# Kernel tuning notes

Hardware: AMD Instinct MI355X
Metric: run time of the kernel (lower is better)

The kernel has to match this reference:

```python
import jax, jax.numpy as jnp
import numpy as np

N = 16384        # num_nodes (64 graphs x 256 nodes, consecutive blocks)
G = 64           # num_graphs = len(nodes_per_graph)
GENES = 12132    # num_genes (hardcoded in source)
E = 262144       # edges, avg degree 16
PER = 256        # nodes per graph


def setup_inputs() -> dict:
    key = jax.random.key(0)
    ks = jax.random.split(key, 12)
    x = jax.random.normal(ks[0], (N, GENES), dtype=jnp.float32)
    edge_index = jax.random.randint(ks[1], (2, E), 0, N, dtype=jnp.int32)
    # node i belongs to graph i // PER  (consecutive-block partition as in the source loop)
    graph_ids = jnp.repeat(jnp.arange(G, dtype=jnp.int32), PER)
    node_scales = jax.random.uniform(ks[2], (GENES,), dtype=jnp.float32, minval=0.5, maxval=1.5)
    gcn_weight = jax.random.normal(ks[3], (GENES, G), dtype=jnp.float32) / np.float32(np.sqrt(GENES))
    gcn_bias = jax.random.normal(ks[4], (G,), dtype=jnp.float32) * 0.01
    w1 = jax.random.normal(ks[5], (G, N), dtype=jnp.float32) / np.float32(np.sqrt(N))   # to_graph_layer [out,in]
    b1 = jax.random.normal(ks[6], (G,), dtype=jnp.float32) * 0.01
    final_means = jax.random.normal(ks[7], (G,), dtype=jnp.float32)
    final_scales = jax.random.uniform(ks[8], (G,), dtype=jnp.float32, minval=0.5, maxval=1.5)
    w2 = jax.random.normal(ks[9], (1, G), dtype=jnp.float32) / np.float32(np.sqrt(G))   # to_final_layer
    b2 = jax.random.normal(ks[10], (1,), dtype=jnp.float32) * 0.01
    return {
        "x": x, "edge_index": edge_index, "graph_ids": graph_ids,
        "node_scales": node_scales, "gcn_weight": gcn_weight, "gcn_bias": gcn_bias,
        "w1": w1, "b1": b1, "final_means": final_means, "final_scales": final_scales,
        "w2": w2, "b2": b2,
    }


def reference(x, edge_index, graph_ids, node_scales, gcn_weight, gcn_bias,
              w1, b1, final_means, final_scales, w2, b2):
    n = x.shape[0]
    x = x / node_scales                              # [N, GENES]
    xw = x @ gcn_weight                              # [N, G]  GCNConv linear (normalize=False)
    src, dst = edge_index[0], edge_index[1]
    # message passing: sum x_j over in-edges; '+ xw' realizes the explicitly-added self loops
    agg = jax.ops.segment_sum(xw[src], dst, num_segments=n) + xw + gcn_bias  # [N, G]
    # per-graph gather: node i takes column graph_ids[i] (vectorized form of the source loop)
    selected = jnp.take_along_axis(agg, graph_ids[:, None], axis=1)[:, 0]    # [N]
    # NOTE: the (selected - graph_means)/graph_scales in the source is dead code
    # (immediately overwritten by `x = selected_outputs`), so it is omitted.
    h = w1 @ selected + b1                           # [G]
    h = (h - final_means) / final_scales
    out = w2 @ h + b2                                # [1]
    return jax.nn.sigmoid(out)
```

## Files before the change

kernel.cpp:

```cpp
#include <hip/hip_runtime.h>
#include <hip/hip_bf16.h>

typedef unsigned short u16;
typedef unsigned int   u32;
typedef __attribute__((ext_vector_type(8))) short bf16x8;
typedef __attribute__((ext_vector_type(4))) float f32x4;
typedef __attribute__((ext_vector_type(4))) u32   u32x4;

#define GENES  12132
#define KPAD   12160
#define NROW   16384
#define GCOL   64
#define KTAIL  12096
#define KSPLIT 10
#define CPW    38

__device__ __forceinline__ u32 pack_hi(float x, float y) {
  return __builtin_amdgcn_perm(__float_as_uint(y), __float_as_uint(x), 0x07060302u);
}
__device__ __forceinline__ u32 pack_lo(float x, float y) {
  float lx = x - __uint_as_float(__float_as_uint(x) & 0xFFFF0000u);
  float ly = y - __uint_as_float(__float_as_uint(y) & 0xFFFF0000u);
  return pack_hi(lx, ly);
}
__device__ __forceinline__ void cvt8v(f32x4 a, f32x4 b, bf16x8& h8, bf16x8& l8) {
  u32x4 hv = { pack_hi(a[0], a[1]), pack_hi(a[2], a[3]),
               pack_hi(b[0], b[1]), pack_hi(b[2], b[3]) };
  u32x4 lv = { pack_lo(a[0], a[1]), pack_lo(a[2], a[3]),
               pack_lo(b[0], b[1]), pack_lo(b[2], b[3]) };
  h8 = __builtin_bit_cast(bf16x8, hv);
  l8 = __builtin_bit_cast(bf16x8, lv);
}

__global__ __launch_bounds__(256) void prep_all(
    const float* __restrict__ gw, const float* __restrict__ ns,
    const float* __restrict__ x,
    u16* __restrict__ B2, float* __restrict__ xpad, float* __restrict__ hbuf) {
  const int bid = blockIdx.x;
  const int t   = threadIdx.x;
  if (bid < KPAD / 64) {
    __shared__ u16 th[64 * 72];
    __shared__ u16 tl[64 * 72];
    const int k0 = bid * 64;
#pragma unroll
    for (int i = 0; i < 16; ++i) {
      int idx = i * 256 + t;
      int k = idx >> 6, c = idx & 63;
      int gk = k0 + k;
      float wv = 0.f;
      if (gk < GENES) wv = gw[(size_t)gk * GCOL + c] / ns[gk];
      u32 u = __float_as_uint(wv);
      float lf = wv - __uint_as_float(u & 0xFFFF0000u);
      th[c * 72 + k] = (u16)(u >> 16);
      tl[c * 72 + k] = (u16)(__float_as_uint(lf) >> 16);
    }
    __syncthreads();
#pragma unroll
    for (int i = 0; i < 4; ++i) {
      int idx = i * 256 + t;
      int ch2 = idx >> 9;
      int cg  = (idx >> 7) & 3;
      int pl  = (idx >> 6) & 1;
      int l   = idx & 63;
      int c   = cg * 16 + (l & 15);
      int klo = ch2 * 32 + (l >> 4) * 8;
      const u16* src = (pl ? tl : th) + c * 72 + klo;
      u16* dst = B2 + ((size_t)((bid * 2 + ch2) * 8 + cg * 2 + pl) * 64 + l) * 8;
      *(uint4*)dst = *(const uint4*)src;
    }
  } else {
    int i = (bid - KPAD / 64) * 256 + t;
    int row = i >> 6, col = i & 63;
    float v = 0.f;
    if (col < GENES - KTAIL) v = x[(size_t)row * GENES + KTAIL + col];
    xpad[i] = v;
    if (bid == KPAD / 64 && t < 64) hbuf[t] = 0.f;
  }
}

__global__ __launch_bounds__(256, 4) void gemm_kernel(
    const float* __restrict__ x, const float* __restrict__ xpad,
    const u16* __restrict__ B2, float* __restrict__ xwp) {
  const int sp = blockIdx.x >> 7;
  const int rg = blockIdx.x & 127;
  const int w  = threadIdx.x >> 6;
  const int l  = threadIdx.x & 63;
  const int lr = l & 15;
  const int kq = l >> 4;
  const int r0 = rg * 128 + w * 32;

  f32x4 acc[2][4];
#pragma unroll
  for (int m = 0; m < 2; ++m)
#pragma unroll
    for (int c = 0; c < 4; ++c) acc[m][c] = (f32x4){0.f, 0.f, 0.f, 0.f};

  const float* a0 = x    + (size_t)(r0 + lr) * GENES + kq * 8;
  const float* p0 = xpad + (size_t)(r0 + lr) * 64    + kq * 8;
  const int c0 = sp * CPW;

  f32x4 an0a, an0b, an1a, an1b;
  auto LOADA = [&](int gch) {
    if (gch < KTAIL / 32) {
      const float* q0 = a0 + gch * 32;
      const float* q1 = q0 + (size_t)16 * GENES;
      an0a = *(const f32x4*)q0;  an0b = *(const f32x4*)(q0 + 4);
      an1a = *(const f32x4*)q1;  an1b = *(const f32x4*)(q1 + 4);
    } else {
      const float* q0 = p0 + (gch * 32 - KTAIL);
      const float* q1 = q0 + 16 * 64;
      an0a = *(const f32x4*)q0;  an0b = *(const f32x4*)(q0 + 4);
      an1a = *(const f32x4*)q1;  an1b = *(const f32x4*)(q1 + 4);
    }
  };

  LOADA(c0);

  for (int ci = 0; ci < CPW; ++ci) {
    const int gch = c0 + ci;
    const u16* bp = B2 + (size_t)gch * 4096 + l * 8;
    bf16x8 bh[4], bl[4];
#pragma unroll
    for (int cg = 0; cg < 4; ++cg) {
      bh[cg] = *(const bf16x8*)(bp + (cg * 2 + 0) * 512);
      bl[cg] = *(const bf16x8*)(bp + (cg * 2 + 1) * 512);
    }
    bf16x8 ah0, al0, ah1, al1;
    cvt8v(an0a, an0b, ah0, al0);
    cvt8v(an1a, an1b, ah1, al1);
    if (ci + 1 < CPW) LOADA(gch + 1);
#pragma unroll
    for (int cg = 0; cg < 4; ++cg) {
      acc[0][cg] = __builtin_amdgcn_mfma_f32_16x16x32_bf16(ah0, bh[cg], acc[0][cg], 0, 0, 0);
      acc[0][cg] = __builtin_amdgcn_mfma_f32_16x16x32_bf16(al0, bh[cg], acc[0][cg], 0, 0, 0);
      acc[0][cg] = __builtin_amdgcn_mfma_f32_16x16x32_bf16(ah0, bl[cg], acc[0][cg], 0, 0, 0);
      acc[1][cg] = __builtin_amdgcn_mfma_f32_16x16x32_bf16(ah1, bh[cg], acc[1][cg], 0, 0, 0);
      acc[1][cg] = __builtin_amdgcn_mfma_f32_16x16x32_bf16(al1, bh[cg], acc[1][cg], 0, 0, 0);
      acc[1][cg] = __builtin_amdgcn_mfma_f32_16x16x32_bf16(ah1, bl[cg], acc[1][cg], 0, 0, 0);
    }
  }

  float* outp = xwp + (size_t)sp * NROW * GCOL;
#pragma unroll
  for (int m = 0; m < 2; ++m) {
    const int rbase = r0 + m * 16 + kq * 4;
#pragma unroll
    for (int cg = 0; cg < 4; ++cg) {
      const int col = cg * 16 + lr;
#pragma unroll
      for (int j = 0; j < 4; ++j)
        outp[(size_t)(rbase + j) * GCOL + col] = acc[m][cg][j];
    }
  }
}

__global__ __launch_bounds__(256) void reduce_sel(
    const f32x4* __restrict__ xwp, f32x4* __restrict__ xw4,
    const float* __restrict__ gb, float* __restrict__ sel) {
  int i = blockIdx.x * 256 + threadIdx.x;
  f32x4 v = xwp[i];
#pragma unroll
  for (int p = 1; p < KSPLIT; ++p) {
    f32x4 u = xwp[(size_t)p * (NROW * GCOL / 4) + i];
    v[0] += u[0]; v[1] += u[1]; v[2] += u[2]; v[3] += u[3];
  }
  xw4[i] = v;
  int row = i >> 4;
  int g = row >> 8;
  if ((i & 15) == (g >> 2)) sel[row] = v[g & 3] + gb[g];
}

__global__ __launch_bounds__(256) void edge_kernel(
    const int* __restrict__ ei, const float* __restrict__ xw,
    float* __restrict__ sel, int E) {
  int e = blockIdx.x * 256 + threadIdx.x;
  if (e < E) {
    int s = ei[e];
    int d = ei[E + e];
    int g = d >> 8;
    atomicAdd(&sel[d], xw[(size_t)s * GCOL + g]);
  }
}

__global__ __launch_bounds__(256) void hreduce_kernel(
    const float* __restrict__ w1, const float* __restrict__ sel,
    float* __restrict__ hbuf) {
  const int k = blockIdx.x >> 2;
  const int q = blockIdx.x & 3;
  const int t = threadIdx.x;
  const float4* wr = reinterpret_cast<const float4*>(w1 + (size_t)k * NROW);
  const float4* sv = reinterpret_cast<const float4*>(sel);
  float sum = 0.f;
#pragma unroll
  for (int i = 0; i < 4; ++i) {
    int idx = q * 1024 + i * 256 + t;
    float4 a = wr[idx];
    float4 b = sv[idx];
    sum += a.x * b.x + a.y * b.y + a.z * b.z + a.w * b.w;
  }
#pragma unroll
  for (int off = 32; off > 0; off >>= 1) sum += __shfl_down(sum, off, 64);
  __shared__ float wsum[4];
  if ((t & 63) == 0) wsum[t >> 6] = sum;
  __syncthreads();
  if (t == 0) atomicAdd(&hbuf[k], wsum[0] + wsum[1] + wsum[2] + wsum[3]);
}

__global__ void finalize_kernel(
    const float* __restrict__ hbuf, const float* __restrict__ b1,
    const float* __restrict__ fm, const float* __restrict__ fs,
    const float* __restrict__ w2, const float* __restrict__ b2,
    float* __restrict__ out) {
  int t = threadIdx.x;
  float h  = hbuf[t] + b1[t];
  float hn = (h - fm[t]) / fs[t];
  float v  = w2[t] * hn;
#pragma unroll
  for (int off = 32; off > 0; off >>= 1) v += __shfl_down(v, off, 64);
  if (t == 0) {
    float z = v + b2[0];
    out[0] = 1.f / (1.f + expf(-z));
  }
}

extern "C" void kernel_launch(void* const* d_in, const int* in_sizes, int n_in,
                              void* d_out, int out_size, void* d_ws, size_t ws_size,
                              hipStream_t stream) {
  const float* x    = (const float*)d_in[0];
  const int*   ei   = (const int*)d_in[1];
  const float* ns   = (const float*)d_in[3];
  const float* gw   = (const float*)d_in[4];
  const float* gb   = (const float*)d_in[5];
  const float* w1   = (const float*)d_in[6];
  const float* b1   = (const float*)d_in[7];
  const float* fm   = (const float*)d_in[8];
  const float* fs   = (const float*)d_in[9];
  const float* w2   = (const float*)d_in[10];
  const float* b2   = (const float*)d_in[11];
  float* out = (float*)d_out;

  const int E = in_sizes[1] / 2;

  float* ws   = (float*)d_ws;
  float* xw   = ws;
  float* sel  = xw + (size_t)NROW * GCOL;
  float* hbuf = sel + NROW;
  u16*   B2   = (u16*)(hbuf + 64);
  float* xpad = (float*)(B2 + (size_t)380 * 4096);
  float* xwp  = xpad + (size_t)NROW * 64;

  hipLaunchKernelGGL(prep_all, dim3(KPAD / 64 + NROW * 64 / 256), dim3(256), 0, stream,
                     gw, ns, x, B2, xpad, hbuf);
  hipLaunchKernelGGL(gemm_kernel, dim3(128 * KSPLIT), dim3(256), 0, stream,
                     x, xpad, B2, xwp);
  hipLaunchKernelGGL(reduce_sel, dim3(NROW * GCOL / 4 / 256), dim3(256), 0, stream,
                     (const f32x4*)xwp, (f32x4*)xw, gb, sel);
  hipLaunchKernelGGL(edge_kernel, dim3((E + 255) / 256), dim3(256), 0, stream,
                     ei, xw, sel, E);
  hipLaunchKernelGGL(hreduce_kernel, dim3(GCOL * 4), dim3(256), 0, stream,
                     w1, sel, hbuf);
  hipLaunchKernelGGL(finalize_kernel, dim3(1), dim3(64), 0, stream,
                     hbuf, b1, fm, fs, w2, b2, out);
}
```

Baseline: 299.7 us.

## Restructure GEMM to stream A tiles via async LDS loads without split-K

```diff
diff --git a/kernel.cpp b/kernel.cpp
--- a/kernel.cpp
+++ b/kernel.cpp
@@ -7,13 +7,13 @@
 typedef __attribute__((ext_vector_type(4))) float f32x4;
 typedef __attribute__((ext_vector_type(4))) u32   u32x4;
 
-#define GENES  12132
-#define KPAD   12160
-#define NROW   16384
-#define GCOL   64
-#define KTAIL  12096
-#define KSPLIT 10
-#define CPW    38
+#define GENES   12132
+#define KPAD    12160
+#define NROW    16384
+#define GCOL    64
+#define BCHUNKS 380
+#define KSTAGES 48
+#define KTAIL2  12032
 
 __device__ __forceinline__ u32 pack_hi(float x, float y) {
   return __builtin_amdgcn_perm(__float_as_uint(y), __float_as_uint(x), 0x07060302u);
@@ -30,6 +30,12 @@
                pack_lo(b[0], b[1]), pack_lo(b[2], b[3]) };
   h8 = __builtin_bit_cast(bf16x8, hv);
   l8 = __builtin_bit_cast(bf16x8, lv);
+}
+
+__device__ __forceinline__ void gload16(const void* g, void* l) {
+  __builtin_amdgcn_global_load_lds(
+      (const __attribute__((address_space(1))) void*)g,
+      (__attribute__((address_space(3))) void*)l, 16, 0, 0);
 }
 
 __global__ __launch_bounds__(256) void prep_all(
@@ -70,104 +76,103 @@
     }
   } else {
     int i = (bid - KPAD / 64) * 256 + t;
-    int row = i >> 6, col = i & 63;
-    float v = 0.f;
-    if (col < GENES - KTAIL) v = x[(size_t)row * GENES + KTAIL + col];
-    xpad[i] = v;
+    int row = i >> 6, q = i & 63;
+    float4 v;
+    float* vp = (float*)&v;
+#pragma unroll
+    for (int j = 0; j < 4; ++j) {
+      int col = q * 4 + j;
+      vp[j] = (col < GENES - KTAIL2) ? x[(size_t)row * GENES + KTAIL2 + col] : 0.f;
+    }
+    ((float4*)xpad)[i] = v;
     if (bid == KPAD / 64 && t < 64) hbuf[t] = 0.f;
   }
 }
 
-__global__ __launch_bounds__(256, 4) void gemm_kernel(
+__global__ __launch_bounds__(256, 3) void gemm_kernel(
     const float* __restrict__ x, const float* __restrict__ xpad,
-    const u16* __restrict__ B2, float* __restrict__ xwp) {
-  const int sp = blockIdx.x >> 7;
-  const int rg = blockIdx.x & 127;
-  const int w  = threadIdx.x >> 6;
-  const int l  = threadIdx.x & 63;
+    const u16* __restrict__ B2, const float* __restrict__ gb,
+    float* __restrict__ xw, float* __restrict__ sel) {
+  __shared__ float Abuf[3][16 * 256];
+
+  const int t  = threadIdx.x;
+  const int w  = t >> 6;
+  const int l  = t & 63;
   const int lr = l & 15;
   const int kq = l >> 4;
-  const int r0 = rg * 128 + w * 32;
-
-  f32x4 acc[2][4];
-#pragma unroll
-  for (int m = 0; m < 2; ++m)
-#pragma unroll
-    for (int c = 0; c < 4; ++c) acc[m][c] = (f32x4){0.f, 0.f, 0.f, 0.f};
-
-  const float* a0 = x    + (size_t)(r0 + lr) * GENES + kq * 8;
-  const float* p0 = xpad + (size_t)(r0 + lr) * 64    + kq * 8;
-  const int c0 = sp * CPW;
-
-  f32x4 an0a, an0b, an1a, an1b;
-  auto LOADA = [&](int gch) {
-    if (gch < KTAIL / 32) {
-      const float* q0 = a0 + gch * 32;
-      const float* q1 = q0 + (size_t)16 * GENES;
-      an0a = *(const f32x4*)q0;  an0b = *(const f32x4*)(q0 + 4);
-      an1a = *(const f32x4*)q1;  an1b = *(const f32x4*)(q1 + 4);
-    } else {
-      const float* q0 = p0 + (gch * 32 - KTAIL);
-      const float* q1 = q0 + 16 * 64;
-      an0a = *(const f32x4*)q0;  an0b = *(const f32x4*)(q0 + 4);
-      an1a = *(const f32x4*)q1;  an1b = *(const f32x4*)(q1 + 4);
+  const int r0 = blockIdx.x * 16;
+
+  f32x4 acc = (f32x4){0.f, 0.f, 0.f, 0.f};
+
+  auto STAGE = [&](int buf, int s) {
+#pragma unroll
+    for (int rr = 0; rr < 4; ++rr) {
+      const int R = 4 * w + rr;
+      const float* src = (s < KSTAGES - 1)
+          ? x    + (size_t)(r0 + R) * GENES + s * 256
+          : xpad + (size_t)(r0 + R) * 256;
+      gload16(src + ((l ^ (R & 7)) << 2), &Abuf[buf][R * 256]);
     }
   };
 
-  LOADA(c0);
-
-  for (int ci = 0; ci < CPW; ++ci) {
-    const int gch = c0 + ci;
-    const u16* bp = B2 + (size_t)gch * 4096 + l * 8;
-    bf16x8 bh[4], bl[4];
-#pragma unroll
-    for (int cg = 0; cg < 4; ++cg) {
-      bh[cg] = *(const bf16x8*)(bp + (cg * 2 + 0) * 512);
-      bl[cg] = *(const bf16x8*)(bp + (cg * 2 + 1) * 512);
-    }
-    bf16x8 ah0, al0, ah1, al1;
-    cvt8v(an0a, an0b, ah0, al0);
-    cvt8v(an1a, an1b, ah1, al1);
-    if (ci + 1 < CPW) LOADA(gch + 1);
-#pragma unroll
-    for (int cg = 0; cg < 4; ++cg) {
-      acc[0][cg] = __builtin_amdgcn_mfma_f32_16x16x32_bf16(ah0, bh[cg], acc[0][cg], 0, 0, 0);
-      acc[0][cg] = __builtin_amdgcn_mfma_f32_16x16x32_bf16(al0, bh[cg], acc[0][cg], 0, 0, 0);
-      acc[0][cg] = __builtin_amdgcn_mfma_f32_16x16x32_bf16(ah0, bl[cg], acc[0][cg], 0, 0, 0);
-      acc[1][cg] = __builtin_amdgcn_mfma_f32_16x16x32_bf16(ah1, bh[cg], acc[1][cg], 0, 0, 0);
-      acc[1][cg] = __builtin_amdgcn_mfma_f32_16x16x32_bf16(al1, bh[cg], acc[1][cg], 0, 0, 0);
-      acc[1][cg] = __builtin_amdgcn_mfma_f32_16x16x32_bf16(ah1, bl[cg], acc[1][cg], 0, 0, 0);
-    }
-  }
-
-  float* outp = xwp + (size_t)sp * NROW * GCOL;
-#pragma unroll
-  for (int m = 0; m < 2; ++m) {
-    const int rbase = r0 + m * 16 + kq * 4;
-#pragma unroll
-    for (int cg = 0; cg < 4; ++cg) {
-      const int col = cg * 16 + lr;
-#pragma unroll
-      for (int j = 0; j < 4; ++j)
-        outp[(size_t)(rbase + j) * GCOL + col] = acc[m][cg][j];
-    }
-  }
-}
-
-__global__ __launch_bounds__(256) void reduce_sel(
-    const f32x4* __restrict__ xwp, f32x4* __restrict__ xw4,
-    const float* __restrict__ gb, float* __restrict__ sel) {
-  int i = blockIdx.x * 256 + threadIdx.x;
-  f32x4 v = xwp[i];
-#pragma unroll
-  for (int p = 1; p < KSPLIT; ++p) {
-    f32x4 u = xwp[(size_t)p * (NROW * GCOL / 4) + i];
-    v[0] += u[0]; v[1] += u[1]; v[2] += u[2]; v[3] += u[3];
-  }
-  xw4[i] = v;
-  int row = i >> 4;
-  int g = row >> 8;
-  if ((i & 15) == (g >> 2)) sel[row] = v[g & 3] + gb[g];
+  STAGE(0, 0);
+  STAGE(1, 1);
+
+  int p = 0;
+  for (int s = 0; s < KSTAGES; ++s) {
+    if (s == KSTAGES - 1)
+      asm volatile("s_waitcnt vmcnt(0)" ::: "memory");
+    else
+      asm volatile("s_waitcnt vmcnt(4)" ::: "memory");
+    __builtin_amdgcn_s_barrier();
+
+    const int nch = (s == KSTAGES - 1) ? 4 : 8;
+
+    bf16x8 bh[8], bl[8];
+#pragma unroll
+    for (int c = 0; c < 8; ++c)
+      if (c < nch) {
+        const u16* bp = B2 + (size_t)(s * 8 + c) * 4096 + (w * 2) * 512 + l * 8;
+        bh[c] = *(const bf16x8*)bp;
+        bl[c] = *(const bf16x8*)(bp + 512);
+      }
+    __builtin_amdgcn_sched_barrier(0);
+
+    if (s + 2 < KSTAGES) {
+      int b2 = p + 2; if (b2 >= 3) b2 -= 3;
+      STAGE(b2, s + 2);
+    }
+
+#pragma unroll
+    for (int c = 0; c < 8; ++c)
+      if (c < nch) {
+        const int g0 = c * 8 + kq * 2;
+        const int s0 = g0 ^ (lr & 7);
+        f32x4 va = *(const f32x4*)&Abuf[p][lr * 256 + s0 * 4];
+        f32x4 vb = *(const f32x4*)&Abuf[p][lr * 256 + (s0 ^ 1) * 4];
+        bf16x8 ah, al;
+        cvt8v(va, vb, ah, al);
+        acc = __builtin_amdgcn_mfma_f32_16x16x32_bf16(ah, bh[c], acc, 0, 0, 0);
+        acc = __builtin_amdgcn_mfma_f32_16x16x32_bf16(al, bh[c], acc, 0, 0, 0);
+        acc = __builtin_amdgcn_mfma_f32_16x16x32_bf16(ah, bl[c], acc, 0, 0, 0);
+      }
+
+    ++p; if (p == 3) p = 0;
+  }
+
+  const int col  = w * 16 + lr;
+  const int rbase = r0 + kq * 4;
+#pragma unroll
+  for (int j = 0; j < 4; ++j)
+    xw[(size_t)(rbase + j) * GCOL + col] = acc[j];
+
+  const int g = blockIdx.x >> 4;
+  if (col == g) {
+    const float bias = gb[g];
+#pragma unroll
+    for (int j = 0; j < 4; ++j)
+      sel[rbase + j] = acc[j] + bias;
+  }
 }
 
 __global__ __launch_bounds__(256) void edge_kernel(
@@ -246,15 +251,12 @@
   float* sel  = xw + (size_t)NROW * GCOL;
   float* hbuf = sel + NROW;
   u16*   B2   = (u16*)(hbuf + 64);
-  float* xpad = (float*)(B2 + (size_t)380 * 4096);
-  float* xwp  = xpad + (size_t)NROW * 64;
+  float* xpad = (float*)(B2 + (size_t)BCHUNKS * 4096);
 
   hipLaunchKernelGGL(prep_all, dim3(KPAD / 64 + NROW * 64 / 256), dim3(256), 0, stream,
                      gw, ns, x, B2, xpad, hbuf);
-  hipLaunchKernelGGL(gemm_kernel, dim3(128 * KSPLIT), dim3(256), 0, stream,
-                     x, xpad, B2, xwp);
-  hipLaunchKernelGGL(reduce_sel, dim3(NROW * GCOL / 4 / 256), dim3(256), 0, stream,
-                     (const f32x4*)xwp, (f32x4*)xw, gb, sel);
+  hipLaunchKernelGGL(gemm_kernel, dim3(NROW / 16), dim3(256), 0, stream,
+                     x, xpad, B2, gb, xw, sel);
   hipLaunchKernelGGL(edge_kernel, dim3((E + 255) / 256), dim3(256), 0, stream,
                      ei, xw, sel, E);
   hipLaunchKernelGGL(hreduce_kernel, dim3(GCOL * 4), dim3(256), 0, stream,
```

Result: faster. 287.5 us (median of 2 runs) (-4.1%).

## Rebalance GEMM split-K to four splits with 64-row tiles and widened tail pad

Applied to the files above, without the earlier changes.

```diff
diff --git a/kernel.cpp b/kernel.cpp
--- a/kernel.cpp
+++ b/kernel.cpp
@@ -7,13 +7,14 @@
 typedef __attribute__((ext_vector_type(4))) float f32x4;
 typedef __attribute__((ext_vector_type(4))) u32   u32x4;
 
-#define GENES  12132
-#define KPAD   12160
-#define NROW   16384
-#define GCOL   64
-#define KTAIL  12096
-#define KSPLIT 10
-#define CPW    38
+#define GENES   12132
+#define KPAD    12288
+#define NCH     384
+#define NROW    16384
+#define GCOL    64
+#define KTAIL2  12032
+#define KSPLIT  4
+#define CPW     96
 
 __device__ __forceinline__ u32 pack_hi(float x, float y) {
   return __builtin_amdgcn_perm(__float_as_uint(y), __float_as_uint(x), 0x07060302u);
@@ -70,10 +71,15 @@
     }
   } else {
     int i = (bid - KPAD / 64) * 256 + t;
-    int row = i >> 6, col = i & 63;
-    float v = 0.f;
-    if (col < GENES - KTAIL) v = x[(size_t)row * GENES + KTAIL + col];
-    xpad[i] = v;
+    int row = i >> 6, q = i & 63;
+    float4 v;
+    float* vp = (float*)&v;
+#pragma unroll
+    for (int j = 0; j < 4; ++j) {
+      int col = q * 4 + j;
+      vp[j] = (col < GENES - KTAIL2) ? x[(size_t)row * GENES + KTAIL2 + col] : 0.f;
+    }
+    ((float4*)xpad)[i] = v;
     if (bid == KPAD / 64 && t < 64) hbuf[t] = 0.f;
   }
 }
@@ -81,76 +87,80 @@
 __global__ __launch_bounds__(256, 4) void gemm_kernel(
     const float* __restrict__ x, const float* __restrict__ xpad,
     const u16* __restrict__ B2, float* __restrict__ xwp) {
-  const int sp = blockIdx.x >> 7;
-  const int rg = blockIdx.x & 127;
+  const int sp = blockIdx.x & 3;
+  const int wg = blockIdx.x >> 2;
   const int w  = threadIdx.x >> 6;
   const int l  = threadIdx.x & 63;
   const int lr = l & 15;
   const int kq = l >> 4;
-  const int r0 = rg * 128 + w * 32;
-
-  f32x4 acc[2][4];
-#pragma unroll
-  for (int m = 0; m < 2; ++m)
-#pragma unroll
-    for (int c = 0; c < 4; ++c) acc[m][c] = (f32x4){0.f, 0.f, 0.f, 0.f};
-
-  const float* a0 = x    + (size_t)(r0 + lr) * GENES + kq * 8;
-  const float* p0 = xpad + (size_t)(r0 + lr) * 64    + kq * 8;
+  const int r0 = wg * 64 + w * 16;
+
+  f32x4 acc[4];
+#pragma unroll
+  for (int c = 0; c < 4; ++c) acc[c] = (f32x4){0.f, 0.f, 0.f, 0.f};
+
+  const float* ax = x    + (size_t)(r0 + lr) * GENES + kq * 8;
+  const float* ap = xpad + (size_t)(r0 + lr) * 256   + kq * 8;
   const int c0 = sp * CPW;
+  const int SW = 376 - c0;
 
   f32x4 an0a, an0b, an1a, an1b;
-  auto LOADA = [&](int gch) {
-    if (gch < KTAIL / 32) {
-      const float* q0 = a0 + gch * 32;
-      const float* q1 = q0 + (size_t)16 * GENES;
-      an0a = *(const f32x4*)q0;  an0b = *(const f32x4*)(q0 + 4);
-      an1a = *(const f32x4*)q1;  an1b = *(const f32x4*)(q1 + 4);
-    } else {
-      const float* q0 = p0 + (gch * 32 - KTAIL);
-      const float* q1 = q0 + 16 * 64;
-      an0a = *(const f32x4*)q0;  an0b = *(const f32x4*)(q0 + 4);
-      an1a = *(const f32x4*)q1;  an1b = *(const f32x4*)(q1 + 4);
-    }
-  };
-
-  LOADA(c0);
-
-  for (int ci = 0; ci < CPW; ++ci) {
-    const int gch = c0 + ci;
-    const u16* bp = B2 + (size_t)gch * 4096 + l * 8;
-    bf16x8 bh[4], bl[4];
-#pragma unroll
-    for (int cg = 0; cg < 4; ++cg) {
-      bh[cg] = *(const bf16x8*)(bp + (cg * 2 + 0) * 512);
-      bl[cg] = *(const bf16x8*)(bp + (cg * 2 + 1) * 512);
-    }
-    bf16x8 ah0, al0, ah1, al1;
-    cvt8v(an0a, an0b, ah0, al0);
-    cvt8v(an1a, an1b, ah1, al1);
-    if (ci + 1 < CPW) LOADA(gch + 1);
-#pragma unroll
-    for (int cg = 0; cg < 4; ++cg) {
-      acc[0][cg] = __builtin_amdgcn_mfma_f32_16x16x32_bf16(ah0, bh[cg], acc[0][cg], 0, 0, 0);
-      acc[0][cg] = __builtin_amdgcn_mfma_f32_16x16x32_bf16(al0, bh[cg], acc[0][cg], 0, 0, 0);
-      acc[0][cg] = __builtin_amdgcn_mfma_f32_16x16x32_bf16(ah0, bl[cg], acc[0][cg], 0, 0, 0);
-      acc[1][cg] = __builtin_amdgcn_mfma_f32_16x16x32_bf16(ah1, bh[cg], acc[1][cg], 0, 0, 0);
-      acc[1][cg] = __builtin_amdgcn_mfma_f32_16x16x32_bf16(al1, bh[cg], acc[1][cg], 0, 0, 0);
-      acc[1][cg] = __builtin_amdgcn_mfma_f32_16x16x32_bf16(ah1, bl[cg], acc[1][cg], 0, 0, 0);
-    }
-  }
+#define LOADA(A, B, ci)                                            \
+  { const float* q = ((ci) < SW) ? ax + (size_t)(c0 + (ci)) * 32   \
+                                 : ap + (size_t)((ci) - SW) * 32;  \
+    A = *(const f32x4*)q;  B = *(const f32x4*)(q + 4); }
+
+  LOADA(an0a, an0b, 0)
+  LOADA(an1a, an1b, 1)
+
+  for (int i = 0; i < CPW; i += 2) {
+    {
+      bf16x8 ah, al;
+      cvt8v(an0a, an0b, ah, al);
+      if (i + 2 < CPW) LOADA(an0a, an0b, i + 2)
+      const u16* bp = B2 + (size_t)(c0 + i) * 4096 + l * 8;
+      bf16x8 bh[4], bl[4];
+#pragma unroll
+      for (int cg = 0; cg < 4; ++cg) {
+        bh[cg] = *(const bf16x8*)(bp + cg * 1024);
+        bl[cg] = *(const bf16x8*)(bp + cg * 1024 + 512);
+      }
+#pragma unroll
+      for (int cg = 0; cg < 4; ++cg) {
+        acc[cg] = __builtin_amdgcn_mfma_f32_16x16x32_bf16(ah, bh[cg], acc[cg], 0, 0, 0);
+        acc[cg] = __builtin_amdgcn_mfma_f32_16x16x32_bf16(al, bh[cg], acc[cg], 0, 0, 0);
+        acc[cg] = __builtin_amdgcn_mfma_f32_16x16x32_bf16(ah, bl[cg], acc[cg], 0, 0, 0);
+      }
+    }
+    {
+      bf16x8 ah, al;
+      cvt8v(an1a, an1b, ah, al);
+      if (i + 3 < CPW) LOADA(an1a, an1b, i + 3)
+      const u16* bp = B2 + (size_t)(c0 + i + 1) * 4096 + l * 8;
+      bf16x8 bh[4], bl[4];
+#pragma unroll
+      for (int cg = 0; cg < 4; ++cg) {
+        bh[cg] = *(const bf16x8*)(bp + cg * 1024);
+        bl[cg] = *(const bf16x8*)(bp + cg * 1024 + 512);
+      }
+#pragma unroll
+      for (int cg = 0; cg < 4; ++cg) {
+        acc[cg] = __builtin_amdgcn_mfma_f32_16x16x32_bf16(ah, bh[cg], acc[cg], 0, 0, 0);
+        acc[cg] = __builtin_amdgcn_mfma_f32_16x16x32_bf16(al, bh[cg], acc[cg], 0, 0, 0);
+        acc[cg] = __builtin_amdgcn_mfma_f32_16x16x32_bf16(ah, bl[cg], acc[cg], 0, 0, 0);
+      }
+    }
+  }
+#undef LOADA
 
   float* outp = xwp + (size_t)sp * NROW * GCOL;
-#pragma unroll
-  for (int m = 0; m < 2; ++m) {
-    const int rbase = r0 + m * 16 + kq * 4;
-#pragma unroll
-    for (int cg = 0; cg < 4; ++cg) {
-      const int col = cg * 16 + lr;
-#pragma unroll
-      for (int j = 0; j < 4; ++j)
-        outp[(size_t)(rbase + j) * GCOL + col] = acc[m][cg][j];
-    }
+  const int rbase = r0 + kq * 4;
+#pragma unroll
+  for (int cg = 0; cg < 4; ++cg) {
+    const int col = cg * 16 + lr;
+#pragma unroll
+    for (int j = 0; j < 4; ++j)
+      outp[(size_t)(rbase + j) * GCOL + col] = acc[cg][j];
   }
 }
 
@@ -246,12 +256,12 @@
   float* sel  = xw + (size_t)NROW * GCOL;
   float* hbuf = sel + NROW;
   u16*   B2   = (u16*)(hbuf + 64);
-  float* xpad = (float*)(B2 + (size_t)380 * 4096);
-  float* xwp  = xpad + (size_t)NROW * 64;
+  float* xpad = (float*)(B2 + (size_t)NCH * 4096);
+  float* xwp  = xpad + (size_t)NROW * 256;
 
   hipLaunchKernelGGL(prep_all, dim3(KPAD / 64 + NROW * 64 / 256), dim3(256), 0, stream,
                      gw, ns, x, B2, xpad, hbuf);
-  hipLaunchKernelGGL(gemm_kernel, dim3(128 * KSPLIT), dim3(256), 0, stream,
+  hipLaunchKernelGGL(gemm_kernel, dim3(256 * KSPLIT), dim3(256), 0, stream,
                      x, xpad, B2, xwp);
   hipLaunchKernelGGL(reduce_sel, dim3(NROW * GCOL / 4 / 256), dim3(256), 0, stream,
                      (const f32x4*)xwp, (f32x4*)xw, gb, sel);
```

Result: slower. 334.8 us (+11.7%).
